# Kernel tuning notes

Hardware: AMD Instinct MI355X
Metric: run time of the kernel (lower is better)

The kernel has to match this reference:

```python
import jax, jax.numpy as jnp
import numpy as np

B, N = 2, 6
H, W = 64, 64            # BEV grid
FH, FW = 32, 88          # camera feature map
DIM, FEAT_DIM = 128, 128
HEADS, DH = 4, 32
QW1, QW2 = 8, 8          # query window
KW1, KW2 = 4, 11         # key/val window
IMG_H, IMG_W = 224, 480
EPS = 1e-5


def _ln(t, g, b):
    m = t.mean(-1, keepdims=True)
    v = ((t - m) ** 2).mean(-1, keepdims=True)
    return (t - m) / jnp.sqrt(v + EPS) * g + b


def _bn_relu_conv(t, g, b, Wc):
    # eval-mode BatchNorm2d (running_mean=0, running_var=1) -> ReLU -> 1x1 conv
    y = jax.nn.relu(t / jnp.sqrt(1.0 + EPS) * g[:, None, None] + b[:, None, None])
    return jnp.einsum('oc,nchw->nohw', Wc, y)


def _normalize(t, axis):
    n = jnp.sqrt(jnp.sum(t * t, axis=axis, keepdims=True))
    return t / jnp.maximum(n, 1e-12)


def _win(t, w1, w2):
    # (..., X*w1, Y*w2, d) -> (..., X, Y, w1, w2, d)
    s = t.shape
    t = t.reshape(*s[:-3], s[-3] // w1, w1, s[-2] // w2, w2, s[-1])
    return jnp.swapaxes(t, -4, -3)


def _unwin(t):
    # (..., X, Y, w1, w2, d) -> (..., X*w1, Y*w2, d)
    s = t.shape
    return jnp.swapaxes(t, -4, -3).reshape(*s[:-5], s[-5] * s[-3], s[-4] * s[-2], s[-1])


def _gridwin(t, w1, w2):
    bb, nn, Ht, Wt, d = t.shape
    t = t.reshape(bb, nn, w1, Ht // w1, w2, Wt // w2, d)
    return t.transpose(0, 1, 3, 5, 2, 4, 6)  # (b, n, X, Y, w1, w2, d)


def _cross_win_attn(qw, kw, vw, ln_g, ln_b, Wqkv, bqkv, Wp, bp, skip):
    b, n, X, Y, w1, w2, d = qw.shape
    f1, f2 = kw.shape[4], kw.shape[5]
    L = X * Y
    q = qw.transpose(0, 2, 3, 1, 4, 5, 6).reshape(b, L, n * w1 * w2, d)
    k = kw.transpose(0, 2, 3, 1, 4, 5, 6).reshape(b, L, n * f1 * f2, d)
    v = vw.transpose(0, 2, 3, 1, 4, 5, 6).reshape(b, L, n * f1 * f2, d)
    q = _ln(q, ln_g[0], ln_b[0]) @ Wqkv[0] + bqkv[0]
    k = _ln(k, ln_g[1], ln_b[1]) @ Wqkv[1] + bqkv[1]
    v = _ln(v, ln_g[2], ln_b[2]) @ Wqkv[2] + bqkv[2]
    split = lambda t: t.reshape(*t.shape[:-1], HEADS, DH)  # head-major channel split
    q, k, v = split(q), split(k), split(v)
    att = jax.nn.softmax(DH ** -0.5 * jnp.einsum('blqhd,blkhd->bhlqk', q, k), axis=-1)
    o = jnp.einsum('bhlqk,blkhd->blqhd', att, v).reshape(b, L, n * w1 * w2, HEADS * DH)
    o = o @ Wp + bp
    o = o.reshape(b, X, Y, n, w1, w2, d).mean(3)  # mean over cameras
    return o + skip


def _forward(x, grid, feature, I_inv, E_inv,
             bn_fl_g, bn_fl_b, W_fl, bn_fp_g, bn_fp_b, W_fp,
             W_bev, b_bev, W_img, W_cam,
             attn_ln_g, attn_ln_b, attn_Wqkv, attn_bqkv, attn_Wp, attn_bp,
             pn_g, pn_b, Wma, bma, Wmb, bmb, post_g, post_b):
    b, n = feature.shape[:2]
    # image plane (buffer)
    xs = jnp.linspace(0.0, 1.0, FW) * IMG_W
    ys = jnp.linspace(0.0, 1.0, FH) * IMG_H
    gx, gy = jnp.meshgrid(xs, ys)  # (FH, FW) each
    plane = jnp.stack([gx, gy, jnp.ones_like(gx)], 0).reshape(3, FH * FW)
    # camera embedding from translation column of E_inv
    c = E_inv[..., -1]                                   # (b, n, 4)
    c_embed = jnp.einsum('oc,bnc->bno', W_cam, c)        # (b, n, dim)
    # unprojected rays
    cam = jnp.einsum('bnij,jk->bnik', I_inv, plane)      # (b, n, 3, HW)
    cam = jnp.concatenate([cam, jnp.ones_like(cam[:, :, :1])], 2)
    d = jnp.einsum('bnij,bnjk->bnik', E_inv, cam)        # (b, n, 4, HW)
    d_img = d.reshape(b, n, 4, FH, FW)
    d_embed = jnp.einsum('oc,bnchw->bnohw', W_img, d_img)
    img_embed = _normalize(d_embed - c_embed[..., None, None], axis=2)
    # BEV positional embedding
    w_embed = jnp.einsum('oc,chw->ohw', W_bev, grid[:2]) + b_bev[:, None, None]
    bev_embed = _normalize(w_embed[None, None] - c_embed[..., None, None], axis=2)  # (b,n,dim,H,W)
    feat = feature.reshape(b * n, FEAT_DIM, FH, FW)
    key_im = img_embed + _bn_relu_conv(feat, bn_fp_g, bn_fp_b, W_fp).reshape(b, n, DIM, FH, FW)
    val_im = _bn_relu_conv(feat, bn_fl_g, bn_fl_b, W_fl).reshape(b, n, DIM, FH, FW)
    query = bev_embed + x[:, None]                       # (b, n, dim, H, W)
    # channel-last
    q_im = query.transpose(0, 1, 3, 4, 2)
    k_im = key_im.transpose(0, 1, 3, 4, 2)
    v_im = val_im.transpose(0, 1, 3, 4, 2)
    x_im = x.transpose(0, 2, 3, 1)
    # stage 1: local windows
    qw = _win(q_im, QW1, QW2)
    kw = _win(k_im, KW1, KW2)
    vw = _win(v_im, KW1, KW2)
    o1 = _cross_win_attn(qw, kw, vw, attn_ln_g[0], attn_ln_b[0], attn_Wqkv[0],
                         attn_bqkv[0], attn_Wp[0], attn_bp[0], _win(x_im, QW1, QW2))
    q1 = _unwin(o1)                                      # (b, H, W, d)
    q1 = q1 + jax.nn.gelu(_ln(q1, pn_g[0], pn_b[0]) @ Wma[0] + bma[0], approximate=False) @ Wmb[0] + bmb[0]
    # stage 2: grid (swapped) windows
    qg = jnp.broadcast_to(q1[:, None], (b, n) + q1.shape[1:])
    o2 = _cross_win_attn(_win(qg, QW1, QW2), _gridwin(k_im, KW1, KW2), _gridwin(v_im, KW1, KW2),
                         attn_ln_g[1], attn_ln_b[1], attn_Wqkv[1], attn_bqkv[1],
                         attn_Wp[1], attn_bp[1], _win(q1, QW1, QW2))
    q2 = _unwin(o2)
    q2 = q2 + jax.nn.gelu(_ln(q2, pn_g[1], pn_b[1]) @ Wma[1] + bma[1], approximate=False) @ Wmb[1] + bmb[1]
    out = _ln(q2, post_g, post_b)
    return out.transpose(0, 3, 1, 2)                     # (b, dim, H, W)


def setup_inputs() -> dict:
    key = jax.random.key(0)
    ks = jax.random.split(key, 16)
    rn = lambda i, shape, sc=0.02: jax.random.normal(ks[i], shape, dtype=jnp.float32) * sc
    return {
        'index': 0,
        'x': jax.random.normal(ks[0], (B, DIM, H, W), dtype=jnp.float32),
        'grid': jax.random.normal(ks[1], (2, H, W), dtype=jnp.float32),
        'feature': jax.random.normal(ks[2], (B, N, FEAT_DIM, FH, FW), dtype=jnp.float32),
        'I_inv': jax.random.normal(ks[3], (B, N, 3, 3), dtype=jnp.float32),
        'E_inv': jax.random.normal(ks[4], (B, N, 4, 4), dtype=jnp.float32),
        'bn_fl_g': jnp.ones((FEAT_DIM,), jnp.float32), 'bn_fl_b': jnp.zeros((FEAT_DIM,), jnp.float32),
        'W_fl': rn(5, (DIM, FEAT_DIM)),
        'bn_fp_g': jnp.ones((FEAT_DIM,), jnp.float32), 'bn_fp_b': jnp.zeros((FEAT_DIM,), jnp.float32),
        'W_fp': rn(6, (DIM, FEAT_DIM)),
        'W_bev': rn(7, (DIM, 2)), 'b_bev': jnp.zeros((DIM,), jnp.float32),
        'W_img': rn(8, (DIM, 4)), 'W_cam': rn(9, (DIM, 4)),
        'attn_ln_g': jnp.ones((2, 3, DIM), jnp.float32), 'attn_ln_b': jnp.zeros((2, 3, DIM), jnp.float32),
        'attn_Wqkv': rn(10, (2, 3, DIM, HEADS * DH)), 'attn_bqkv': jnp.zeros((2, 3, HEADS * DH), jnp.float32),
        'attn_Wp': rn(11, (2, HEADS * DH, DIM)), 'attn_bp': jnp.zeros((2, DIM), jnp.float32),
        'pn_g': jnp.ones((2, DIM), jnp.float32), 'pn_b': jnp.zeros((2, DIM), jnp.float32),
        'Wma': rn(12, (2, DIM, 2 * DIM)), 'bma': jnp.zeros((2, 2 * DIM), jnp.float32),
        'Wmb': rn(13, (2, 2 * DIM, DIM)), 'bmb': jnp.zeros((2, DIM), jnp.float32),
        'post_g': jnp.ones((DIM,), jnp.float32), 'post_b': jnp.zeros((DIM,), jnp.float32),
    }


def reference(index, x, grid, feature, I_inv, E_inv,
              bn_fl_g, bn_fl_b, W_fl, bn_fp_g, bn_fp_b, W_fp,
              W_bev, b_bev, W_img, W_cam,
              attn_ln_g, attn_ln_b, attn_Wqkv, attn_bqkv, attn_Wp, attn_bp,
              pn_g, pn_b, Wma, bma, Wmb, bmb, post_g, post_b):
    del index  # grid for this index is passed directly
    return _forward(x, grid, feature, I_inv, E_inv,
                    bn_fl_g, bn_fl_b, W_fl, bn_fp_g, bn_fp_b, W_fp,
                    W_bev, b_bev, W_img, W_cam,
                    attn_ln_g, attn_ln_b, attn_Wqkv, attn_bqkv, attn_Wp, attn_bp,
                    pn_g, pn_b, Wma, bma, Wmb, bmb, post_g, post_b)
```

## Files before the change

### kernel.cpp

```cpp
#include <hip/hip_runtime.h>
#include <math.h>


typedef __attribute__((ext_vector_type(8))) short short8;
typedef __attribute__((ext_vector_type(4))) float f32x4;

__device__ __forceinline__ unsigned short f2bf(float f){
  union { float f; unsigned u; } v; v.f = f;
  unsigned r = v.u + 0x7FFF + ((v.u >> 16) & 1);
  return (unsigned short)(r >> 16);
}
__device__ __forceinline__ float bf2f(unsigned short h){
  union { unsigned u; float f; } v; v.u = ((unsigned)h) << 16; return v.f;
}
__device__ __forceinline__ void store_bf16x8(unsigned short* p, const float* v){
  union { short8 s8; unsigned short u[8]; } u;
  #pragma unroll
  for (int i=0;i<8;i++) u.u[i] = f2bf(v[i]);
  *(short8*)p = u.s8;
}

__device__ __forceinline__ float gelu_erf(float x){
  float z = x * 0.70710678118654752f;
  float a = fabsf(z);
  float t = 1.0f / fmaf(0.3275911f, a, 1.0f);
  float p = t*(0.254829592f + t*(-0.284496736f + t*(1.421413741f +
            t*(-1.453152027f + t*1.061405429f))));
  float er = 1.0f - p*__expf(-a*a);
  er = copysignf(er, z);
  return 0.5f * x * (1.0f + er);
}

__device__ __forceinline__ size_t remap_kv(int tok, int mode){
  int bn = tok / 2816; int p = tok - bn*2816;
  int b = bn / 6, n = bn - b*6;
  int i = p / 88, j = p - i*88;
  int l, t;
  if (mode == 1){
    int jw = j / 11;
    l = (i >> 2)*8 + jw;
    t = n*44 + (i & 3)*11 + (j - jw*11);
  } else {
    l = (i & 7)*8 + (j & 7);
    t = n*44 + (i >> 3)*11 + (j >> 3);
  }
  return (size_t)((b*64 + l)*264 + t);
}

__global__ __launch_bounds__(128) void k_prep(
    const float* __restrict__ qkv, const float* __restrict__ wp,
    const float* __restrict__ wma, const float* __restrict__ wmb,
    const float* __restrict__ wfl, const float* __restrict__ wfp,
    unsigned short* __restrict__ Wt,
    const float* __restrict__ Iinv, const float* __restrict__ Einv,
    const float* __restrict__ Wimg, const float* __restrict__ Wcam,
    unsigned short* __restrict__ K1h,
    const float* __restrict__ gridp, const float* __restrict__ Wbev,
    const float* __restrict__ bbev, const float* __restrict__ x,
    const float* __restrict__ lg, const float* __restrict__ lb,
    const float* __restrict__ abqkv, float* __restrict__ biasP,
    unsigned short* __restrict__ Qh){
  __shared__ float sx[128][9];
  int bid = blockIdx.x;
  if (bid < 64){
    const int sel[16]  = {0,0,0,0,0,0, 1,1, 2,2, 3,3,3,3, 4,5};
    const int soff[16] = {0,16384,32768,49152,65536,81920, 0,16384, 0,32768,
                          0,16384,32768,49152, 0,0};
    const int doff[16] = {0,16384,32768,49152,65536,81920, 98304,114688,
                          131072,163840, 196608,212992,229376,245760, 262144,278528};
    const int Ns[16]   = {128,128,128,128,128,128, 128,128, 256,256,
                          128,128,128,128, 128,128};
    const int trs[16]  = {1,1,1,1,1,1, 1,1, 1,1, 1,1,1,1, 0,0};
    int sg = bid >> 2, q = bid & 3;
    const float* srcs[6] = {qkv, wp, wma, wmb, wfl, wfp};
    const float* src = srcs[sel[sg]] + soff[sg];
    unsigned short* dst = Wt + doff[sg];
    int K = 128, N = Ns[sg];
    int quarter = (K*N) >> 2;
    bool fold = (sg >= 1 && sg <= 5);
    const float* gv = lg + sg*128;
    for (int idx = q*quarter + threadIdx.x; idx < (q+1)*quarter; idx += 128){
      int n = idx / K, k = idx - n*K;
      float v = trs[sg] ? src[k*N + n] : src[idx];
      if (fold) v *= gv[k];
      dst[idx] = f2bf(v);
    }
  } else if (bid < 70){
    int m = bid - 64;
    int n = threadIdx.x;
    float s = abqkv[m*128 + n];
    if (m > 0){
      const float* lnb = lb + m*128;
      const float* W = qkv + m*16384;
      for (int k=0;k<128;k++) s = fmaf(lnb[k], W[k*128 + n], s);
    }
    biasP[m*128 + n] = s;
  } else if (bid < 4294){
    int tile = bid - 70;
    int bn = tile / 352; int p0 = (tile - bn*352)*8;
    int xid = threadIdx.x >> 4, part = threadIdx.x & 15;
    int p = p0 + xid;
    int i = p / 88, j = p - i*88;
    float xs = (float)j * (480.0f/87.0f);
    float ys = (float)i * (224.0f/31.0f);
    const float* I = Iinv + bn*9;
    const float* E = Einv + bn*16;
    float c0 = I[0]*xs + I[1]*ys + I[2];
    float c1 = I[3]*xs + I[4]*ys + I[5];
    float c2 = I[6]*xs + I[7]*ys + I[8];
    float d0 = E[0]*c0 + E[1]*c1 + E[2]*c2 + E[3];
    float d1 = E[4]*c0 + E[5]*c1 + E[6]*c2 + E[7];
    float d2 = E[8]*c0 + E[9]*c1 + E[10]*c2 + E[11];
    float d3 = E[12]*c0 + E[13]*c1 + E[14]*c2 + E[15];
    float v[8]; float sq = 0.f;
    #pragma unroll
    for (int k=0;k<8;k++){
      int o = part*8 + k;
      const float* W = Wimg + o*4;
      const float* Wc = Wcam + o*4;
      float de = W[0]*d0 + W[1]*d1 + W[2]*d2 + W[3]*d3;
      float ce = Wc[0]*E[3] + Wc[1]*E[7] + Wc[2]*E[11] + Wc[3]*E[15];
      float vv = de - ce;
      v[k] = vv; sq = fmaf(vv, vv, sq);
    }
    #pragma unroll
    for (int off=8; off>0; off>>=1) sq += __shfl_xor(sq, off, 16);
    float rn = 1.0f / fmaxf(sqrtf(sq), 1e-12f);
    float o8[8];
    #pragma unroll
    for (int k=0;k<8;k++) o8[k] = v[k]*rn;
    store_bf16x8(K1h + (size_t)(bn*2816 + p)*128 + part*8, o8);
  } else {
    int bid2 = bid - 4294;
    int b = bid2 >> 9; int pp0 = (bid2 & 511) << 3;
    {
      int cg = threadIdx.x >> 3, px = threadIdx.x & 7;
      #pragma unroll
      for (int i=0;i<8;i++){
        int c = cg + 16*i;
        sx[c][px] = x[(size_t)b*524288 + (size_t)c*4096 + pp0 + px];
      }
    }
    __syncthreads();
    int xid = threadIdx.x >> 4, part = threadIdx.x & 15;
    int pix = pp0 + xid;
    int h = pix >> 6, w = pix & 63;
    int l = (h>>3)*8 + (w>>3);
    int tq = (h&7)*8 + (w&7);
    float g0 = gridp[pix], g1 = gridp[4096 + pix];
    float we[8], xv[8];
    #pragma unroll
    for (int k=0;k<8;k++){
      int o = part*8 + k;
      we[k] = Wbev[o*2]*g0 + Wbev[o*2+1]*g1 + bbev[o];
      xv[k] = sx[part*8+k][xid];
    }
    for (int n=0; n<6; n++){
      const float* E = Einv + (b*6+n)*16;
      float v[8]; float sq = 0.f;
      #pragma unroll
      for (int k=0;k<8;k++){
        int o = part*8 + k;
        const float* Wc = Wcam + o*4;
        float ce = Wc[0]*E[3] + Wc[1]*E[7] + Wc[2]*E[11] + Wc[3]*E[15];
        float vv = we[k] - ce;
        v[k] = vv; sq = fmaf(vv, vv, sq);
      }
      #pragma unroll
      for (int off=8; off>0; off>>=1) sq += __shfl_xor(sq, off, 16);
      float rn = 1.0f / fmaxf(sqrtf(sq), 1e-12f);
      float q[8]; float s=0.f, s2=0.f;
      #pragma unroll
      for (int k=0;k<8;k++){
        q[k] = fmaf(v[k], rn, xv[k]);
        s += q[k]; s2 = fmaf(q[k], q[k], s2);
      }
      #pragma unroll
      for (int off=8; off>0; off>>=1){ s += __shfl_xor(s, off, 16); s2 += __shfl_xor(s2, off, 16); }
      float mean = s*(1.f/128.f);
      float rstd = rsqrtf(fmaxf(s2*(1.f/128.f) - mean*mean, 0.f) + 1e-5f);
      size_t row = (size_t)((b*64 + l)*384 + n*64 + tq);
      float o8[8];
      #pragma unroll
      for (int k=0;k<8;k++){
        int c = part*8 + k;
        o8[k] = fmaf((q[k]-mean)*rstd, lg[c], lb[c]);
      }
      store_bf16x8(Qh + row*128 + part*8, o8);
    }
  }
}

__global__ __launch_bounds__(256) void k_conv(const float* __restrict__ feat,
    const float* __restrict__ gK, const float* __restrict__ bK,
    const unsigned short* __restrict__ WK, unsigned short* __restrict__ K1h,
    const float* __restrict__ gV, const float* __restrict__ bV,
    const unsigned short* __restrict__ WV, unsigned short* __restrict__ V1h){
  constexpr int KP_ = 136;
  __shared__ unsigned short sW[128*KP_];
  __shared__ unsigned short sA[128*KP_];
  __shared__ float sg[128], sb[128];
  __shared__ float sMean[128], sRstd[128];
  const int which = (blockIdx.x >= 264);
  const int bid = which ? blockIdx.x - 264 : blockIdx.x;
  const float* gg = which ? gV : gK;
  const float* bb = which ? bV : bK;
  const unsigned short* Wts = which ? WV : WK;
  unsigned short* OUT = which ? V1h : K1h;
  const int tid = threadIdx.x;
  const int base = bid * 128;
  for (int i = tid; i < 2048; i += 256){
    int n = i >> 4, k8 = (i & 15) << 3;
    *(short8*)&sW[n*KP_ + k8] = *(const short8*)(Wts + (size_t)n*128 + k8);
  }
  if (tid < 128){ sg[tid]=gg[tid]; sb[tid]=bb[tid]; }
  const float RSQ = rsqrtf(1.0f + 1e-5f);
  {
    int prow = tid & 127, cseg = tid >> 7;
    int bn = base / 2816;
    int p = base - bn*2816 + prow;
    const float* fb = feat + ((size_t)bn*128 + cseg*64)*2816 + p;
    #pragma unroll 8
    for (int i=0;i<64;i+=2){
      int c = cseg*64 + i;
      float t0 = fb[(size_t)i*2816] * RSQ;
      float t1 = fb[(size_t)(i+1)*2816] * RSQ;
      float y0 = fmaxf(fmaf(t0, sg[c],   sb[c]),   0.f);
      float y1 = fmaxf(fmaf(t1, sg[c+1], sb[c+1]), 0.f);
      unsigned u = (unsigned)f2bf(y0) | ((unsigned)f2bf(y1) << 16);
      *(unsigned*)&sA[prow*KP_ + c] = u;
    }
  }
  __syncthreads();
  const int lane = tid & 63, wv = tid >> 6;
  const int lane15 = lane & 15, quad = lane >> 4;
  const int n0 = wv * 32;
  f32x4 acc[8][2];
  #pragma unroll
  for (int mt=0; mt<8; mt++){ acc[mt][0]=(f32x4)0.f; acc[mt][1]=(f32x4)0.f; }
  const unsigned short* aptr = sA + lane15*KP_ + quad*8;
  const unsigned short* bptr = sW + (size_t)(n0 + lane15)*KP_ + quad*8;
  #pragma unroll
  for (int kk=0; kk<4; kk++){
    short8 af[8], bf2v[2];
    #pragma unroll
    for (int mt=0; mt<8; mt++) af[mt] = *(const short8*)(aptr + mt*16*KP_ + kk*32);
    bf2v[0] = *(const short8*)(bptr + kk*32);
    bf2v[1] = *(const short8*)(bptr + 16*KP_ + kk*32);
    #pragma unroll
    for (int mt=0; mt<8; mt++){
      acc[mt][0] = __builtin_amdgcn_mfma_f32_16x16x32_bf16(af[mt], bf2v[0], acc[mt][0], 0,0,0);
      acc[mt][1] = __builtin_amdgcn_mfma_f32_16x16x32_bf16(af[mt], bf2v[1], acc[mt][1], 0,0,0);
    }
  }
  __syncthreads();
  #pragma unroll
  for (int mt=0; mt<8; mt++){
    #pragma unroll
    for (int nt=0; nt<2; nt++){
      int col = n0 + nt*16 + lane15;
      #pragma unroll
      for (int r4=0; r4<4; r4++){
        int row = mt*16 + quad*4 + r4;
        float v = acc[mt][nt][r4];
        if (!which) v += bf2f(K1h[(size_t)(base+row)*128 + col]);
        sA[row*KP_ + col] = f2bf(v);
      }
    }
  }
  __syncthreads();
  {
    int r = tid >> 1, part = tid & 1;
    float s=0.f, s2=0.f;
    #pragma unroll 8
    for (int k=0;k<64;k++){
      float v = bf2f(sA[r*KP_ + part*64 + k]);
      s += v; s2 = fmaf(v,v,s2);
    }
    s += __shfl_xor(s, 1); s2 += __shfl_xor(s2, 1);
    if (part == 0){
      float mean = s*(1.f/128.f);
      sMean[r] = mean;
      sRstd[r] = rsqrtf(fmaxf(s2*(1.f/128.f) - mean*mean, 0.f) + 1e-5f);
    }
  }
  __syncthreads();
  for (int i = tid; i < 2048; i += 256){
    int row = i >> 4, seg = i & 15;
    float mean = sMean[row], rstd = sRstd[row];
    union { short8 s; unsigned short u[8]; } t;
    t.s = *(const short8*)&sA[row*KP_ + seg*8];
    float v[8];
    #pragma unroll
    for (int k=0;k<8;k++) v[k] = (bf2f(t.u[k]) - mean)*rstd;
    store_bf16x8(OUT + (size_t)(base+row)*128 + seg*8, v);
  }
}

struct GArg {
  const unsigned short* Xh;
  const unsigned short* Wt; const float* bias;
  unsigned short* OUTH; float oscale; int outmode;
};

__global__ __launch_bounds__(256) void k_qkv(GArg ga, GArg gb, GArg gc,
                                             int s1, int s2){
  constexpr int KP_ = 136;
  __shared__ unsigned short sW[128*KP_];
  __shared__ unsigned short sA[128*KP_];
  __shared__ float sbias[128];
  const int b0 = (int)blockIdx.x;
  const GArg g = (b0 < s1) ? ga : (b0 < s2) ? gb : gc;
  const int bid = (b0 < s1) ? b0 : (b0 < s2) ? b0 - s1 : b0 - s2;
  const int base = bid * 128;
  const int tid = threadIdx.x;
  for (int i = tid; i < 2048; i += 256){
    int n = i >> 4, k8 = (i & 15) << 3;
    *(short8*)&sW[n*KP_ + k8] = *(const short8*)(g.Wt + (size_t)n*128 + k8);
  }
  if (tid < 128) sbias[tid] = g.bias[tid];
  {
    const int r = tid >> 1, part = tid & 1;
    const short8* src = (const short8*)(g.Xh + (size_t)(base+r)*128 + part*64);
    short8* dst = (short8*)(sA + r*KP_ + part*64);
    #pragma unroll
    for (int k=0;k<8;k++) dst[k] = src[k];
  }
  __syncthreads();
  const int lane = tid & 63, wv = tid >> 6;
  const int lane15 = lane & 15, quad = lane >> 4;
  const int n0 = wv * 32;
  f32x4 acc[8][2];
  #pragma unroll
  for (int mt=0; mt<8; mt++){ acc[mt][0]=(f32x4)0.f; acc[mt][1]=(f32x4)0.f; }
  const unsigned short* aptr = sA + lane15*KP_ + quad*8;
  const unsigned short* bptr = sW + (size_t)(n0 + lane15)*KP_ + quad*8;
  #pragma unroll
  for (int kk=0; kk<4; kk++){
    short8 af[8], bf2v[2];
    #pragma unroll
    for (int mt=0; mt<8; mt++) af[mt] = *(const short8*)(aptr + mt*16*KP_ + kk*32);
    bf2v[0] = *(const short8*)(bptr + kk*32);
    bf2v[1] = *(const short8*)(bptr + 16*KP_ + kk*32);
    #pragma unroll
    for (int mt=0; mt<8; mt++){
      acc[mt][0] = __builtin_amdgcn_mfma_f32_16x16x32_bf16(af[mt], bf2v[0], acc[mt][0], 0,0,0);
      acc[mt][1] = __builtin_amdgcn_mfma_f32_16x16x32_bf16(af[mt], bf2v[1], acc[mt][1], 0,0,0);
    }
  }
  __syncthreads();
  #pragma unroll
  for (int mt=0; mt<8; mt++){
    #pragma unroll
    for (int nt=0; nt<2; nt++){
      int col = n0 + nt*16 + lane15;
      float bsv = sbias[col];
      #pragma unroll
      for (int r4=0; r4<4; r4++){
        int row = mt*16 + quad*4 + r4;
        sA[row*KP_ + col] = f2bf((acc[mt][nt][r4] + bsv) * g.oscale);
      }
    }
  }
  __syncthreads();
  for (int i = tid; i < 2048; i += 256){
    int row = i >> 4, seg = i & 15;
    int rrow = base + row;
    size_t orow = g.outmode ? remap_kv(rrow, g.outmode) : (size_t)rrow;
    *(short8*)(g.OUTH + orow*128 + seg*8) = *(const short8*)&sA[row*KP_ + seg*8];
  }
}

__global__ __launch_bounds__(256) void k_tail(
    const unsigned short* __restrict__ AOh,
    const float* __restrict__ skipf, int skipmode,
    const unsigned short* __restrict__ WtP, const float* __restrict__ abp,
    const float* __restrict__ png, const float* __restrict__ pnb,
    const unsigned short* __restrict__ WtMAa, const unsigned short* __restrict__ WtMAb,
    const float* __restrict__ bma,
    const unsigned short* __restrict__ WtMBa, const unsigned short* __restrict__ WtMBb,
    const float* __restrict__ bmb,
    float* __restrict__ Q1out, unsigned short* __restrict__ Q1n,
    const float* __restrict__ postg, const float* __restrict__ postb,
    float* __restrict__ out){
  constexpr int KP_ = 136;
  __shared__ unsigned short sW[128*KP_];
  __shared__ unsigned short sX[32*KP_];
  __shared__ unsigned short sH1[32*KP_];
  __shared__ unsigned short sH2[32*KP_];
  __shared__ float sCUR[32*132];
  __shared__ float sbias[128];
  __shared__ float sg[128], sb2[128];
  __shared__ float sMean[32], sRstd[32];
  const int tid = threadIdx.x;
  const int base = blockIdx.x * 32;
  const int lane = tid & 63, wv = tid >> 6;
  const int lane15 = lane & 15, quad = lane >> 4;
  const int n0 = wv * 32;

  auto loadW = [&](const unsigned short* Wp){
    for (int i = tid; i < 2048; i += 256){
      int n = i >> 4, k8 = (i & 15) << 3;
      *(short8*)&sW[n*KP_ + k8] = *(const short8*)(Wp + (size_t)n*128 + k8);
    }
  };
  auto domfma = [&](const unsigned short* Asrc, f32x4 acc[2][2]){
    const unsigned short* aptr = Asrc + lane15*KP_ + quad*8;
    const unsigned short* bptr = sW + (size_t)(n0 + lane15)*KP_ + quad*8;
    #pragma unroll
    for (int kk=0; kk<4; kk++){
      short8 a0 = *(const short8*)(aptr + kk*32);
      short8 a1 = *(const short8*)(aptr + 16*KP_ + kk*32);
      short8 b0 = *(const short8*)(bptr + kk*32);
      short8 b1 = *(const short8*)(bptr + 16*KP_ + kk*32);
      acc[0][0] = __builtin_amdgcn_mfma_f32_16x16x32_bf16(a0,b0,acc[0][0],0,0,0);
      acc[1][0] = __builtin_amdgcn_mfma_f32_16x16x32_bf16(a1,b0,acc[1][0],0,0,0);
      acc[0][1] = __builtin_amdgcn_mfma_f32_16x16x32_bf16(a0,b1,acc[0][1],0,0,0);
      acc[1][1] = __builtin_amdgcn_mfma_f32_16x16x32_bf16(a1,b1,acc[1][1],0,0,0);
    }
  };

  loadW(WtP);
  {
    const int r = tid >> 3, part = tid & 7;
    const short8* src = (const short8*)(AOh + (size_t)(base+r)*128 + part*16);
    short8* dst = (short8*)(sX + r*KP_ + part*16);
    dst[0] = src[0]; dst[1] = src[1];
  }
  if (tid < 128){ sbias[tid] = abp[tid]; sg[tid] = png[tid]; sb2[tid] = pnb[tid]; }
  __syncthreads();
  {
    f32x4 acc[2][2];
    acc[0][0]=(f32x4)0.f; acc[0][1]=(f32x4)0.f;
    acc[1][0]=(f32x4)0.f; acc[1][1]=(f32x4)0.f;
    domfma(sX, acc);
    #pragma unroll
    for (int mt=0; mt<2; mt++)
      #pragma unroll
      for (int nt=0; nt<2; nt++){
        int col = n0 + nt*16 + lane15;
        float bsv = sbias[col];
        #pragma unroll
        for (int r4=0; r4<4; r4++){
          int row = mt*16 + quad*4 + r4;
          int rrow = base + row;
          float v = acc[mt][nt][r4] + bsv;
          if (skipmode == 1){
            int bb = rrow >> 12, l = (rrow >> 6) & 63, pp = rrow & 63;
            int pix = (((l>>3)*8 + (pp>>3)) << 6) + (l&7)*8 + (pp&7);
            v += skipf[(size_t)bb*524288 + (size_t)col*4096 + pix];
          } else {
            v += skipf[(size_t)rrow*128 + col];
          }
          sCUR[row*132 + col] = v;
        }
      }
  }
  __syncthreads();
  loadW(WtMAa);
  if (tid < 128) sbias[tid] = bma[tid];
  {
    const int r = tid >> 3, part = tid & 7;
    float v[16];
    #pragma unroll
    for (int k=0;k<16;k++) v[k] = sCUR[r*132 + part*16 + k];
    float s=0.f, s2=0.f;
    #pragma unroll
    for (int k=0;k<16;k++){ s += v[k]; s2 = fmaf(v[k],v[k],s2); }
    #pragma unroll
    for (int off=4; off>0; off>>=1){ s += __shfl_xor(s, off, 8); s2 += __shfl_xor(s2, off, 8); }
    float mean = s*(1.f/128.f);
    float rstd = rsqrtf(fmaxf(s2*(1.f/128.f) - mean*mean, 0.f) + 1e-5f);
    #pragma unroll
    for (int k=0;k<16;k++){
      int c = part*16 + k;
      v[k] = fmaf((v[k]-mean)*rstd, sg[c], sb2[c]);
    }
    store_bf16x8(sX + r*KP_ + part*16, v);
    store_bf16x8(sX + r*KP_ + part*16 + 8, v+8);
  }
  __syncthreads();
  {
    f32x4 acc[2][2];
    acc[0][0]=(f32x4)0.f; acc[0][1]=(f32x4)0.f;
    acc[1][0]=(f32x4)0.f; acc[1][1]=(f32x4)0.f;
    domfma(sX, acc);
    #pragma unroll
    for (int mt=0; mt<2; mt++)
      #pragma unroll
      for (int nt=0; nt<2; nt++){
        int col = n0 + nt*16 + lane15;
        float bsv = sbias[col];
        #pragma unroll
        for (int r4=0; r4<4; r4++){
          int row = mt*16 + quad*4 + r4;
          sH1[row*KP_ + col] = f2bf(gelu_erf(acc[mt][nt][r4] + bsv));
        }
      }
  }
  __syncthreads();
  loadW(WtMAb);
  if (tid < 128) sbias[tid] = bma[128 + tid];
  __syncthreads();
  {
    f32x4 acc[2][2];
    acc[0][0]=(f32x4)0.f; acc[0][1]=(f32x4)0.f;
    acc[1][0]=(f32x4)0.f; acc[1][1]=(f32x4)0.f;
    domfma(sX, acc);
    #pragma unroll
    for (int mt=0; mt<2; mt++)
      #pragma unroll
      for (int nt=0; nt<2; nt++){
        int col = n0 + nt*16 + lane15;
        float bsv = sbias[col];
        #pragma unroll
        for (int r4=0; r4<4; r4++){
          int row = mt*16 + quad*4 + r4;
          sH2[row*KP_ + col] = f2bf(gelu_erf(acc[mt][nt][r4] + bsv));
        }
      }
  }
  __syncthreads();
  loadW(WtMBa);
  if (tid < 128) sbias[tid] = bmb[tid];
  __syncthreads();
  f32x4 acc[2][2];
  acc[0][0]=(f32x4)0.f; acc[0][1]=(f32x4)0.f;
  acc[1][0]=(f32x4)0.f; acc[1][1]=(f32x4)0.f;
  domfma(sH1, acc);
  __syncthreads();
  loadW(WtMBb);
  __syncthreads();
  domfma(sH2, acc);
  if (out == nullptr){
    #pragma unroll
    for (int mt=0; mt<2; mt++)
      #pragma unroll
      for (int nt=0; nt<2; nt++){
        int col = n0 + nt*16 + lane15;
        float bsv = sbias[col];
        #pragma unroll
        for (int r4=0; r4<4; r4++){
          int row = mt*16 + quad*4 + r4;
          float v = acc[mt][nt][r4] + bsv + sCUR[row*132 + col];
          sCUR[row*132 + col] = v;
          Q1out[(size_t)(base+row)*128 + col] = v;
        }
      }
    __syncthreads();
    {
      const int r = tid >> 3, part = tid & 7;
      float s=0.f, s2=0.f;
      #pragma unroll
      for (int k=0;k<16;k++){
        float v = sCUR[r*132 + part*16 + k];
        s += v; s2 = fmaf(v,v,s2);
      }
      #pragma unroll
      for (int off=4; off>0; off>>=1){ s += __shfl_xor(s, off, 8); s2 += __shfl_xor(s2, off, 8); }
      if (part == 0){
        float mean = s*(1.f/128.f);
        sMean[r] = mean;
        sRstd[r] = rsqrtf(fmaxf(s2*(1.f/128.f) - mean*mean, 0.f) + 1e-5f);
      }
    }
    __syncthreads();
    for (int i = tid; i < 512; i += 256){
      int row = i >> 4, seg = i & 15;
      float mean = sMean[row], rstd = sRstd[row];
      float v[8];
      #pragma unroll
      for (int k=0;k<8;k++) v[k] = (sCUR[row*132 + seg*8 + k] - mean)*rstd;
      store_bf16x8(Q1n + (size_t)(base+row)*128 + seg*8, v);
    }
  } else {
    float res[2][2][4];
    #pragma unroll
    for (int mt=0; mt<2; mt++)
      #pragma unroll
      for (int nt=0; nt<2; nt++){
        int col = n0 + nt*16 + lane15;
        float bsv = sbias[col];
        #pragma unroll
        for (int r4=0; r4<4; r4++){
          int row = mt*16 + quad*4 + r4;
          res[mt][nt][r4] = acc[mt][nt][r4] + bsv + sCUR[row*132 + col];
        }
      }
    __syncthreads();
    #pragma unroll
    for (int mt=0; mt<2; mt++)
      #pragma unroll
      for (int nt=0; nt<2; nt++){
        int col = n0 + nt*16 + lane15;
        #pragma unroll
        for (int r4=0; r4<4; r4++){
          int row = mt*16 + quad*4 + r4;
          sCUR[row*132 + col] = res[mt][nt][r4];
        }
      }
    __syncthreads();
    {
      const int r = tid >> 3, part = tid & 7;
      float s=0.f, s2=0.f;
      #pragma unroll
      for (int k=0;k<16;k++){
        float v = sCUR[r*132 + part*16 + k];
        s += v; s2 = fmaf(v,v,s2);
      }
      #pragma unroll
      for (int off=4; off>0; off>>=1){ s += __shfl_xor(s, off, 8); s2 += __shfl_xor(s2, off, 8); }
      if (part == 0){
        float mean = s*(1.f/128.f);
        sMean[r] = mean;
        sRstd[r] = rsqrtf(fmaxf(s2*(1.f/128.f) - mean*mean, 0.f) + 1e-5f);
      }
    }
    __syncthreads();
    {
      int c = tid & 127, half = tid >> 7;
      int b = base >> 12, l = (base >> 6) & 63, p0 = base & 63;
      float go = postg[c], bo = postb[c];
      #pragma unroll
      for (int seg=0; seg<2; seg++){
        int p = p0 + half*16 + seg*8;
        int hrow = (l>>3)*8 + (p>>3);
        int w0 = (l&7)*8;
        float rr[8];
        #pragma unroll
        for (int j=0;j<8;j++){
          int row = half*16 + seg*8 + j;
          rr[j] = fmaf((sCUR[row*132 + c] - sMean[row])*sRstd[row], go, bo);
        }
        size_t obase = ((size_t)(b*128 + c))*4096 + (size_t)hrow*64 + w0;
        *(float4*)&out[obase]   = make_float4(rr[0],rr[1],rr[2],rr[3]);
        *(float4*)&out[obase+4] = make_float4(rr[4],rr[5],rr[6],rr[7]);
      }
    }
  }
}

__global__ __launch_bounds__(256) void k_attn2(const unsigned short* __restrict__ QPh,
    const unsigned short* __restrict__ KPh, const unsigned short* __restrict__ VPh,
    unsigned short* __restrict__ AOh, int nrep, int nQ){
  __shared__ unsigned short Ksh[288*40];
  __shared__ unsigned short Vt[32*296];
  __shared__ unsigned short Psh[4*16*40];
  __shared__ float rs[4*16];
  int hd = blockIdx.x & 3; int bl = blockIdx.x >> 2;
  size_t kvbase = (size_t)bl*264;
  int tid = threadIdx.x;
  for (int idx = tid; idx < 1056; idx += 256){
    int row = idx >> 2, seg = idx & 3;
    *(short8*)&Ksh[row*40 + seg*8] =
      *(const short8*)(KPh + (kvbase+row)*128 + hd*32 + seg*8);
  }
  for (int idx = tid; idx < 96; idx += 256){
    int row = 264 + (idx>>2), seg = idx & 3;
    short8 z = {0,0,0,0,0,0,0,0};
    *(short8*)&Ksh[row*40 + seg*8] = z;
  }
  for (int idx = tid; idx < 1056; idx += 256){
    int row = idx >> 2, seg = idx & 3;
    union { short8 s; unsigned short u[8]; } t;
    t.s = *(const short8*)(VPh + (kvbase+row)*128 + hd*32 + seg*8);
    #pragma unroll
    for (int i=0;i<8;i++) Vt[(seg*8+i)*296 + row] = t.u[i];
  }
  for (int idx = tid; idx < 384; idx += 256){
    int d = idx / 12, kp = 264 + (idx % 12)*2;
    *(unsigned*)&Vt[d*296 + kp] = 0u;
  }
  __syncthreads();
  const int wv = tid >> 6, lane = tid & 63;
  const int lane15 = lane & 15, quad = lane >> 4;
  unsigned short* Pw = Psh + wv*640;
  float* rsw = rs + wv*16;
  short8 vfrag[9][2];
  #pragma unroll
  for (int kc=0; kc<9; kc++){
    vfrag[kc][0] = *(const short8*)&Vt[(lane15)*296      + kc*32 + quad*8];
    vfrag[kc][1] = *(const short8*)&Vt[(16+lane15)*296   + kc*32 + quad*8];
  }
  f32x4 macc0 = (f32x4)0.f, macc1 = (f32x4)0.f;
  for (int cam = 0; cam < nrep; cam++){
    int qrow = bl*nQ + (cam*4 + wv)*16 + lane15;
    short8 qf = *(const short8*)(QPh + (size_t)qrow*128 + hd*32 + quad*8);
    f32x4 oa0 = (f32x4)0.f, oa1 = (f32x4)0.f;
    float rsum = 0.f;
    #pragma unroll
    for (int kc=0; kc<9; kc++){
      #pragma unroll
      for (int sub=0; sub<2; sub++){
        int kt = kc*2 + sub;
        short8 kf = *(const short8*)&Ksh[(kt*16 + lane15)*40 + quad*8];
        f32x4 st = __builtin_amdgcn_mfma_f32_16x16x32_bf16(kf, qf, (f32x4)0.f, 0,0,0);
        int kbase = kt*16 + quad*4;
        float e0 = (kbase+0 < 264) ? __expf(st[0]) : 0.f;
        float e1 = (kbase+1 < 264) ? __expf(st[1]) : 0.f;
        float e2 = (kbase+2 < 264) ? __expf(st[2]) : 0.f;
        float e3 = (kbase+3 < 264) ? __expf(st[3]) : 0.f;
        rsum += (e0+e1)+(e2+e3);
        uint2 pk;
        pk.x = (unsigned)f2bf(e0) | ((unsigned)f2bf(e1) << 16);
        pk.y = (unsigned)f2bf(e2) | ((unsigned)f2bf(e3) << 16);
        *(uint2*)&Pw[lane15*40 + sub*16 + quad*4] = pk;
      }
      short8 pf = *(const short8*)&Pw[lane15*40 + quad*8];
      oa0 = __builtin_amdgcn_mfma_f32_16x16x32_bf16(pf, vfrag[kc][0], oa0, 0,0,0);
      oa1 = __builtin_amdgcn_mfma_f32_16x16x32_bf16(pf, vfrag[kc][1], oa1, 0,0,0);
    }
    rsum += __shfl_xor(rsum, 16);
    rsum += __shfl_xor(rsum, 32);
    if (lane < 16) rsw[lane] = rsum;
    f32x4 rv = *(f32x4*)&rsw[quad*4];
    #pragma unroll
    for (int r=0;r<4;r++){
      float inv = 1.f / rv[r];
      macc0[r] = fmaf(oa0[r], inv, macc0[r]);
      macc1[r] = fmaf(oa1[r], inv, macc1[r]);
    }
  }
  float sc = (nrep == 6) ? (1.f/6.f) : 1.f;
  int pixb = wv*16 + quad*4;
  #pragma unroll
  for (int r=0;r<4;r++){
    size_t rowo = ((size_t)(bl*64 + pixb + r))*128 + hd*32;
    AOh[rowo + lane15]      = f2bf(macc0[r]*sc);
    AOh[rowo + 16 + lane15] = f2bf(macc1[r]*sc);
  }
}

extern "C" void kernel_launch(void* const* d_in, const int* in_sizes, int n_in,
                              void* d_out, int out_size, void* d_ws, size_t ws_size,
                              hipStream_t stream) {
  (void)in_sizes; (void)n_in; (void)out_size; (void)ws_size;
  const float* x     = (const float*)d_in[1];
  const float* gridp = (const float*)d_in[2];
  const float* feat  = (const float*)d_in[3];
  const float* Iinv  = (const float*)d_in[4];
  const float* Einv  = (const float*)d_in[5];
  const float* gfl   = (const float*)d_in[6];
  const float* bfl   = (const float*)d_in[7];
  const float* Wfl   = (const float*)d_in[8];
  const float* gfp   = (const float*)d_in[9];
  const float* bfp   = (const float*)d_in[10];
  const float* Wfp   = (const float*)d_in[11];
  const float* Wbev  = (const float*)d_in[12];
  const float* bbev  = (const float*)d_in[13];
  const float* Wimg  = (const float*)d_in[14];
  const float* Wcam  = (const float*)d_in[15];
  const float* alng  = (const float*)d_in[16];
  const float* alnb  = (const float*)d_in[17];
  const float* aWqkv = (const float*)d_in[18];
  const float* abqkv = (const float*)d_in[19];
  const float* aWp   = (const float*)d_in[20];
  const float* abp   = (const float*)d_in[21];
  const float* png   = (const float*)d_in[22];
  const float* pnb   = (const float*)d_in[23];
  const float* Wma   = (const float*)d_in[24];
  const float* bma   = (const float*)d_in[25];
  const float* Wmb   = (const float*)d_in[26];
  const float* bmb   = (const float*)d_in[27];
  const float* postg = (const float*)d_in[28];
  const float* postb = (const float*)d_in[29];
  float* out = (float*)d_out;
  float* ws  = (float*)d_ws;
  const float QSC = 0.17677669529663687f;

  float* biasP = ws;
  unsigned short* Wt  = (unsigned short*)(ws + 2048);
  unsigned short* K1h = (unsigned short*)(ws + 149504);
  unsigned short* V1h = K1h + 4325376;
  unsigned short* KPh = V1h + 4325376;
  unsigned short* VPh = KPh + 4325376;
  unsigned short* QPh = VPh + 4325376;
  unsigned short* Qbh = QPh + 6291456;
  unsigned short* AOh = Qbh + 6291456;
  float* Q1f = (float*)(AOh + 1048576);
  unsigned short* Q1n = (unsigned short*)(Q1f + 1048576);

  unsigned short* WtQ1 = Wt;            unsigned short* WtK1 = Wt + 16384;
  unsigned short* WtV1 = Wt + 32768;    unsigned short* WtQ2 = Wt + 49152;
  unsigned short* WtK2 = Wt + 65536;    unsigned short* WtV2 = Wt + 81920;
  unsigned short* WtP1 = Wt + 98304;    unsigned short* WtP2 = Wt + 114688;
  unsigned short* WtMA1 = Wt + 131072;  unsigned short* WtMA2 = Wt + 163840;
  unsigned short* WtMB1a = Wt + 196608; unsigned short* WtMB1b = Wt + 212992;
  unsigned short* WtMB2a = Wt + 229376; unsigned short* WtMB2b = Wt + 245760;
  unsigned short* WtFL = Wt + 262144;   unsigned short* WtFP = Wt + 278528;

  k_prep<<<5318, 128, 0, stream>>>(aWqkv, aWp, Wma, Wmb, Wfl, Wfp, Wt,
      Iinv, Einv, Wimg, Wcam, K1h, gridp, Wbev, bbev, x, alng, alnb,
      abqkv, biasP, Qbh);

  k_conv<<<528, 256, 0, stream>>>(feat, gfp, bfp, WtFP, K1h,
                                  gfl, bfl, WtFL, V1h);

  {
    GArg q{Qbh, WtQ1, biasP,      QPh, QSC, 0};
    GArg kk{K1h, WtK1, biasP+128, KPh, 1.f, 1};
    GArg vv{V1h, WtV1, biasP+256, VPh, 1.f, 1};
    k_qkv<<<912, 256, 0, stream>>>(q, kk, vv, 384, 648);
  }
  k_attn2<<<512, 256, 0, stream>>>(QPh, KPh, VPh, AOh, 6, 384);
  k_tail<<<256, 256, 0, stream>>>(AOh, x, 1, WtP1, abp, png, pnb,
      WtMA1, WtMA1+16384, bma, WtMB1a, WtMB1b, bmb, Q1f, Q1n,
      nullptr, nullptr, nullptr);
  {
    GArg q{Q1n, WtQ2, biasP+384,  QPh, QSC, 0};
    GArg kk{K1h, WtK2, biasP+512, KPh, 1.f, 2};
    GArg vv{V1h, WtV2, biasP+640, VPh, 1.f, 2};
    k_qkv<<<592, 256, 0, stream>>>(q, kk, vv, 64, 328);
  }
  k_attn2<<<512, 256, 0, stream>>>(QPh, KPh, VPh, AOh, 1, 64);
  k_tail<<<256, 256, 0, stream>>>(AOh, Q1f, 3, WtP2, abp+128, png+128, pnb+128,
      WtMA2, WtMA2+16384, bma+256, WtMB2a, WtMB2b, bmb+128, nullptr, nullptr,
      postg, postb, out);
}
```

Baseline: 279.0 us.

## Merge layer-2 K/V projections into first QKV launch and fuse Q2 into tail

```diff
diff --git a/kernel.cpp b/kernel.cpp
--- a/kernel.cpp
+++ b/kernel.cpp
@@ -302,16 +302,18 @@
   const unsigned short* Wt; const float* bias;
   unsigned short* OUTH; float oscale; int outmode;
 };
-
-__global__ __launch_bounds__(256) void k_qkv(GArg ga, GArg gb, GArg gc,
-                                             int s1, int s2){
+struct G5 { GArg g[5]; int s[4]; };
+
+__global__ __launch_bounds__(256) void k_qkv5(G5 A){
   constexpr int KP_ = 136;
   __shared__ unsigned short sW[128*KP_];
   __shared__ unsigned short sA[128*KP_];
   __shared__ float sbias[128];
   const int b0 = (int)blockIdx.x;
-  const GArg g = (b0 < s1) ? ga : (b0 < s2) ? gb : gc;
-  const int bid = (b0 < s1) ? b0 : (b0 < s2) ? b0 - s1 : b0 - s2;
+  const int ridx = (b0 < A.s[0]) ? 0 : (b0 < A.s[1]) ? 1 : (b0 < A.s[2]) ? 2
+                 : (b0 < A.s[3]) ? 3 : 4;
+  const GArg g = A.g[ridx];
+  const int bid = b0 - (ridx ? A.s[ridx-1] : 0);
   const int base = bid * 128;
   const int tid = threadIdx.x;
   for (int i = tid; i < 2048; i += 256){
@@ -380,7 +382,9 @@
     const float* __restrict__ bma,
     const unsigned short* __restrict__ WtMBa, const unsigned short* __restrict__ WtMBb,
     const float* __restrict__ bmb,
-    float* __restrict__ Q1out, unsigned short* __restrict__ Q1n,
+    float* __restrict__ Q1out,
+    const unsigned short* __restrict__ WtQ2, const float* __restrict__ q2bias,
+    float q2scale, unsigned short* __restrict__ QPout,
     const float* __restrict__ postg, const float* __restrict__ postb,
     float* __restrict__ out){
   constexpr int KP_ = 136;
@@ -565,13 +569,38 @@
       }
     }
     __syncthreads();
+    {
+      const int r = tid >> 3, part = tid & 7;
+      float mean = sMean[r], rstd = sRstd[r];
+      float v[16];
+      #pragma unroll
+      for (int k=0;k<16;k++) v[k] = (sCUR[r*132 + part*16 + k] - mean)*rstd;
+      store_bf16x8(sX + r*KP_ + part*16, v);
+      store_bf16x8(sX + r*KP_ + part*16 + 8, v+8);
+    }
+    loadW(WtQ2);
+    if (tid < 128) sbias[tid] = q2bias[tid];
+    __syncthreads();
+    f32x4 a2[2][2];
+    a2[0][0]=(f32x4)0.f; a2[0][1]=(f32x4)0.f;
+    a2[1][0]=(f32x4)0.f; a2[1][1]=(f32x4)0.f;
+    domfma(sX, a2);
+    #pragma unroll
+    for (int mt=0; mt<2; mt++)
+      #pragma unroll
+      for (int nt=0; nt<2; nt++){
+        int col = n0 + nt*16 + lane15;
+        float bsv = sbias[col];
+        #pragma unroll
+        for (int r4=0; r4<4; r4++){
+          int row = mt*16 + quad*4 + r4;
+          sH1[row*KP_ + col] = f2bf((a2[mt][nt][r4] + bsv) * q2scale);
+        }
+      }
+    __syncthreads();
     for (int i = tid; i < 512; i += 256){
       int row = i >> 4, seg = i & 15;
-      float mean = sMean[row], rstd = sRstd[row];
-      float v[8];
-      #pragma unroll
-      for (int k=0;k<8;k++) v[k] = (sCUR[row*132 + seg*8 + k] - mean)*rstd;
-      store_bf16x8(Q1n + (size_t)(base+row)*128 + seg*8, v);
+      *(short8*)(QPout + (size_t)(base+row)*128 + seg*8) = *(const short8*)&sH1[row*KP_ + seg*8];
     }
   } else {
     float res[2][2][4];
@@ -660,12 +689,14 @@
     short8 z = {0,0,0,0,0,0,0,0};
     *(short8*)&Ksh[row*40 + seg*8] = z;
   }
-  for (int idx = tid; idx < 1056; idx += 256){
-    int row = idx >> 2, seg = idx & 3;
-    union { short8 s; unsigned short u[8]; } t;
-    t.s = *(const short8*)(VPh + (kvbase+row)*128 + hd*32 + seg*8);
-    #pragma unroll
-    for (int i=0;i<8;i++) Vt[(seg*8+i)*296 + row] = t.u[i];
+  for (int idx = tid; idx < 528; idx += 256){
+    int kp = idx >> 2, seg = idx & 3;
+    union { short8 s; unsigned short u[8]; } a, b;
+    a.s = *(const short8*)(VPh + (kvbase + 2*kp)*128 + hd*32 + seg*8);
+    b.s = *(const short8*)(VPh + (kvbase + 2*kp + 1)*128 + hd*32 + seg*8);
+    #pragma unroll
+    for (int i=0;i<8;i++)
+      *(unsigned*)&Vt[(seg*8+i)*296 + 2*kp] = (unsigned)a.u[i] | ((unsigned)b.u[i] << 16);
   }
   for (int idx = tid; idx < 384; idx += 256){
     int d = idx / 12, kp = 264 + (idx % 12)*2;
@@ -769,16 +800,17 @@
   const float QSC = 0.17677669529663687f;
 
   float* biasP = ws;
-  unsigned short* Wt  = (unsigned short*)(ws + 2048);
-  unsigned short* K1h = (unsigned short*)(ws + 149504);
-  unsigned short* V1h = K1h + 4325376;
-  unsigned short* KPh = V1h + 4325376;
-  unsigned short* VPh = KPh + 4325376;
-  unsigned short* QPh = VPh + 4325376;
-  unsigned short* Qbh = QPh + 6291456;
-  unsigned short* AOh = Qbh + 6291456;
+  unsigned short* Wt   = (unsigned short*)(ws + 2048);
+  unsigned short* K1h  = (unsigned short*)(ws + 149504);
+  unsigned short* V1h  = K1h + 4325376;
+  unsigned short* KPh  = V1h + 4325376;
+  unsigned short* VPh  = KPh + 4325376;
+  unsigned short* KP2h = VPh + 4325376;
+  unsigned short* VP2h = KP2h + 4325376;
+  unsigned short* QPh  = VP2h + 4325376;
+  unsigned short* Qbh  = QPh + 6291456;
+  unsigned short* AOh  = Qbh + 6291456;
   float* Q1f = (float*)(AOh + 1048576);
-  unsigned short* Q1n = (unsigned short*)(Q1f + 1048576);
 
   unsigned short* WtQ1 = Wt;            unsigned short* WtK1 = Wt + 16384;
   unsigned short* WtV1 = Wt + 32768;    unsigned short* WtQ2 = Wt + 49152;
@@ -797,23 +829,23 @@
                                   gfl, bfl, WtFL, V1h);
 
   {
-    GArg q{Qbh, WtQ1, biasP,      QPh, QSC, 0};
-    GArg kk{K1h, WtK1, biasP+128, KPh, 1.f, 1};
-    GArg vv{V1h, WtV1, biasP+256, VPh, 1.f, 1};
-    k_qkv<<<912, 256, 0, stream>>>(q, kk, vv, 384, 648);
+    G5 A;
+    A.g[0] = GArg{Qbh, WtQ1, biasP,      QPh,  QSC, 0};
+    A.g[1] = GArg{K1h, WtK1, biasP+128,  KPh,  1.f, 1};
+    A.g[2] = GArg{V1h, WtV1, biasP+256,  VPh,  1.f, 1};
+    A.g[3] = GArg{K1h, WtK2, biasP+512,  KP2h, 1.f, 2};
+    A.g[4] = GArg{V1h, WtV2, biasP+640,  VP2h, 1.f, 2};
+    A.s[0] = 384; A.s[1] = 648; A.s[2] = 912; A.s[3] = 1176;
+    k_qkv5<<<1440, 256, 0, stream>>>(A);
   }
   k_attn2<<<512, 256, 0, stream>>>(QPh, KPh, VPh, AOh, 6, 384);
   k_tail<<<256, 256, 0, stream>>>(AOh, x, 1, WtP1, abp, png, pnb,
-      WtMA1, WtMA1+16384, bma, WtMB1a, WtMB1b, bmb, Q1f, Q1n,
+      WtMA1, WtMA1+16384, bma, WtMB1a, WtMB1b, bmb, Q1f,
+      WtQ2, biasP+384, QSC, QPh,
       nullptr, nullptr, nullptr);
-  {
-    GArg q{Q1n, WtQ2, biasP+384,  QPh, QSC, 0};
-    GArg kk{K1h, WtK2, biasP+512, KPh, 1.f, 2};
-    GArg vv{V1h, WtV2, biasP+640, VPh, 1.f, 2};
-    k_qkv<<<592, 256, 0, stream>>>(q, kk, vv, 64, 328);
-  }
-  k_attn2<<<512, 256, 0, stream>>>(QPh, KPh, VPh, AOh, 1, 64);
+  k_attn2<<<512, 256, 0, stream>>>(QPh, KP2h, VP2h, AOh, 1, 64);
   k_tail<<<256, 256, 0, stream>>>(AOh, Q1f, 3, WtP2, abp+128, png+128, pnb+128,
-      WtMA2, WtMA2+16384, bma+256, WtMB2a, WtMB2b, bmb+128, nullptr, nullptr,
+      WtMA2, WtMA2+16384, bma+256, WtMB2a, WtMB2b, bmb+128, nullptr,
+      nullptr, nullptr, 0.f, nullptr,
       postg, postb, out);
 }
```

Measured after the change: 273.1 us. -2.1%, faster.
